# Performance work log

Hardware: AMD Instinct MI355X
Metric: run time of the kernel (lower is better)

Reference implementation:

```python
import jax, jax.numpy as jnp
import numpy as np

T, B, F_, H, D, C = 16, 1024, 512, 128, 8, 100  # trees, batch, feat, hidden, depth, classes
L = 2 ** (D + 1)  # n_leaf = 512


def _routing_tables():
    # Static per-leaf routing: node index and branch side at each depth.
    # Derived from compute_mu's gather indices:
    #   node(d, l) = 2^d - 1 + l // 2^(D+1-d);  side(d, l) = (l // 2^(D-d)) % 2
    l = np.arange(L)
    node = np.stack([(2 ** d - 1) + l // (2 ** (D + 1 - d)) for d in range(D + 1)])  # [D+1, L]
    side = np.stack([(l // (2 ** (D - d))) % 2 for d in range(D + 1)])               # [D+1, L]
    return jnp.asarray(node, dtype=jnp.int32), jnp.asarray(side.astype(np.bool_))


def setup_inputs() -> dict:
    key = jax.random.key(0)
    ks = jax.random.split(key, 4)
    return {
        "feat": jax.random.normal(ks[0], (B, F_), jnp.float32),
        "W1": jax.random.normal(ks[1], (T, F_, H), jnp.float32) * 0.05,
        "b1": jnp.zeros((T, H), jnp.float32),
        "W2": jax.random.normal(ks[2], (T, H, L), jnp.float32) * 0.05,
        "b2": jnp.zeros((T, L), jnp.float32),
        "pi": jax.random.uniform(ks[3], (T, L, C), jnp.float32, -2.0, 2.0),
    }


def reference(feat, W1, b1, W2, b2, pi):
    node, side = _routing_tables()
    # Per-tree MLP head (dropout is identity in eval mode).
    h = jax.nn.relu(jnp.einsum('bf,tfh->tbh', feat, W1) + b1[:, None, :])        # [T,B,H]
    p = jax.nn.sigmoid(jnp.einsum('tbh,thl->tbl', h, W2) + b2[:, None, :])       # [T,B,L]
    # compute_mu: product of routing probs along each root->leaf path.
    sel = p[:, :, node]                          # [T,B,D+1,L] gather (static indices)
    route = jnp.where(side, 1.0 - sel, sel)      # left -> p, right -> 1-p
    mu = jnp.prod(route, axis=2)                 # [T,B,L]
    # compute_py_x: mean over leaves then mean over trees of mu @ softmax(pi).
    leaf_p = jax.nn.softmax(pi, axis=-1)         # [T,L,C]
    py_x = jnp.einsum('tbl,tlc->bc', mu, leaf_p) / (L * T)  # [B,C]
    return jnp.log(py_x)
```

## Files before the change

### kernel.cpp

```cpp
#include <hip/hip_runtime.h>
#include <hip/hip_bf16.h>
#include <math.h>

#define T_ 16
#define B_ 1024
#define F_ 512
#define H_ 128
#define D_ 8
#define C_ 100
#define L_ 512
#define CP_ 112

typedef __attribute__((ext_vector_type(8))) short bf16x8_t;
typedef __attribute__((ext_vector_type(4))) float f32x4_t;

__device__ inline ushort f2bf(float x) {
  __hip_bfloat16 b = __float2bfloat16(x);
  return *(ushort*)&b;
}
__device__ inline float bf2f(ushort u) {
  union { unsigned int i; float f; } v;
  v.i = ((unsigned int)u) << 16;
  return v.f;
}

__device__ inline void bar_raw() {
  asm volatile("" ::: "memory");
  __builtin_amdgcn_s_barrier();
  asm volatile("" ::: "memory");
}
__device__ inline void bar_publish_lds() {
  asm volatile("s_waitcnt lgkmcnt(0)" ::: "memory");
  __builtin_amdgcn_s_barrier();
  asm volatile("" ::: "memory");
}

__global__ __launch_bounds__(256) void k_prep(
    const float* __restrict__ feat, const float* __restrict__ W1,
    const float* __restrict__ W2, const float* __restrict__ pi,
    ushort* __restrict__ feat_bf, ushort* __restrict__ W1T,
    ushort* __restrict__ W2T, ushort* __restrict__ lpT) {
  __shared__ ushort ubuf[112 * 48];
  float (*tile)[33] = (float(*)[33])ubuf;
  ushort (*tileT)[48] = (ushort(*)[48])ubuf;
  const int bid = blockIdx.x, tid = threadIdx.x;

  if (bid < 256) {
    int i = (bid * 256 + tid) * 8;
    float4 a = *(const float4*)(feat + i);
    float4 b = *(const float4*)(feat + i + 4);
    bf16x8_t o;
    o[0] = (short)f2bf(a.x); o[1] = (short)f2bf(a.y);
    o[2] = (short)f2bf(a.z); o[3] = (short)f2bf(a.w);
    o[4] = (short)f2bf(b.x); o[5] = (short)f2bf(b.y);
    o[6] = (short)f2bf(b.z); o[7] = (short)f2bf(b.w);
    *(bf16x8_t*)(feat_bf + i) = o;
    return;
  }
  if (bid < 2304) {
    const float* X; ushort* XT; int K, N, kb, nb, s;
    if (bid < 1280) {
      int r = bid - 256;  kb = r & 15; nb = (r >> 4) & 3;  s = r >> 6;
      X = W1; XT = W1T; K = F_; N = H_;
    } else {
      int r = bid - 1280; kb = r & 3;  nb = (r >> 2) & 15; s = r >> 6;
      X = W2; XT = W2T; K = H_; N = L_;
    }
    const int k0 = kb * 32, n0 = nb * 32;
    const int c = tid & 31, r0 = tid >> 5;
    const float* Xs = X + (size_t)s * K * N;
    ushort* XTs = XT + (size_t)s * N * K;
#pragma unroll
    for (int j = 0; j < 4; ++j)
      tile[r0 + 8 * j][c] = Xs[(size_t)(k0 + r0 + 8 * j) * N + n0 + c];
    __syncthreads();
#pragma unroll
    for (int j = 0; j < 4; ++j)
      XTs[(size_t)(n0 + r0 + 8 * j) * K + k0 + c] = f2bf(tile[c][r0 + 8 * j]);
    return;
  }
  {
    int bid2 = bid - 2304;
    int t = bid2 >> 4, l0 = (bid2 & 15) << 5;
    int lane = tid & 63;
#pragma unroll
    for (int p = 0; p < 8; ++p) {
      int rl = p * 4 + (tid >> 6);
      const float* x = pi + (size_t)(t * L_ + l0 + rl) * C_;
      float v0 = (lane < C_) ? x[lane] : -1e30f;
      float v1 = (lane + 64 < C_) ? x[lane + 64] : -1e30f;
      float m = fmaxf(v0, v1);
#pragma unroll
      for (int off = 32; off; off >>= 1) m = fmaxf(m, __shfl_xor(m, off, 64));
      float e0 = __expf(v0 - m);
      float e1 = (lane + 64 < C_) ? __expf(v1 - m) : 0.0f;
      float sm = e0 + e1;
#pragma unroll
      for (int off = 32; off; off >>= 1) sm += __shfl_xor(sm, off, 64);
      float inv = 1.0f / sm;
      if (lane < C_) tileT[lane][rl] = f2bf(e0 * inv);
      int c2 = lane + 64;
      if (c2 < CP_) tileT[c2][rl] = f2bf(c2 < C_ ? e1 * inv : 0.0f);
    }
    __syncthreads();
    ushort* dst = lpT + (size_t)t * CP_ * L_ + l0;
    for (int idx = tid; idx < 448; idx += 256) {
      int c = idx >> 2, ch = (idx & 3) * 8;
      *(bf16x8_t*)(dst + (size_t)c * L_ + ch) = *(const bf16x8_t*)&tileT[c][ch];
    }
  }
}

__global__ __launch_bounds__(256) void k12_mfma(
    const ushort* __restrict__ feat, const ushort* __restrict__ W1T,
    const float* __restrict__ b1, const ushort* __restrict__ W2T,
    const float* __restrict__ b2, const ushort* __restrict__ lpT,
    float* __restrict__ part) {
  __shared__ ushort smem[29696];
  ushort (*h_s)[136] = (ushort(*)[136])smem;
  ushort (*a_s)[72]  = (ushort(*)[72])(smem + 4352);
  ushort (*b_s)[72]  = (ushort(*)[72])(smem + 6656);
  ushort (*w_s)[136] = (ushort(*)[136])(smem + 4352);
  ushort (*p_s)[520] = (ushort(*)[520])(smem + 13056);

  const int bid = blockIdx.x;
  const int t = bid & 15, b0 = (bid >> 4) * 32;
  const int tid = threadIdx.x;
  const int w = tid >> 6, lane = tid & 63, quad = lane >> 4, n = lane & 15;

  const int arow = tid >> 3, acol = (tid & 7) * 8;
  const ushort* featp = feat + (size_t)(b0 + arow) * F_ + acol;
  const ushort* w1p   = W1T + ((size_t)t * H_ + arow) * F_ + acol;

  {
    f32x4_t acc[2][2];
#pragma unroll
    for (int i = 0; i < 2; ++i)
#pragma unroll
      for (int j = 0; j < 2; ++j) acc[i][j] = (f32x4_t){0.f, 0.f, 0.f, 0.f};

    bf16x8_t ra[2], rb[2][4];
    ra[0] = *(const bf16x8_t*)(featp);
#pragma unroll
    for (int i = 0; i < 4; ++i)
      rb[0][i] = *(const bf16x8_t*)(w1p + (size_t)i * 32 * F_);
    *(bf16x8_t*)&a_s[arow][acol] = ra[0];
#pragma unroll
    for (int i = 0; i < 4; ++i)
      *(bf16x8_t*)&b_s[i * 32 + arow][acol] = rb[0][i];
    bar_publish_lds();
    ra[1] = *(const bf16x8_t*)(featp + 64);
#pragma unroll
    for (int i = 0; i < 4; ++i)
      rb[1][i] = *(const bf16x8_t*)(w1p + (size_t)i * 32 * F_ + 64);
    ra[0] = *(const bf16x8_t*)(featp + 128);
#pragma unroll
    for (int i = 0; i < 4; ++i)
      rb[0][i] = *(const bf16x8_t*)(w1p + (size_t)i * 32 * F_ + 128);

#pragma unroll
    for (int kc = 0; kc < 8; ++kc) {
#pragma unroll
      for (int ks = 0; ks < 64; ks += 32) {
        bf16x8_t af[2], bfr[2];
#pragma unroll
        for (int mt = 0; mt < 2; ++mt)
          af[mt] = *(const bf16x8_t*)&a_s[mt * 16 + n][ks + quad * 8];
#pragma unroll
        for (int nt = 0; nt < 2; ++nt)
          bfr[nt] = *(const bf16x8_t*)&b_s[w * 32 + nt * 16 + n][ks + quad * 8];
#pragma unroll
        for (int mt = 0; mt < 2; ++mt)
#pragma unroll
          for (int nt = 0; nt < 2; ++nt)
            acc[mt][nt] = __builtin_amdgcn_mfma_f32_16x16x32_bf16(
                af[mt], bfr[nt], acc[mt][nt], 0, 0, 0);
      }
      bar_raw();
      if (kc < 7) {
        const int p = (kc + 1) & 1;
        *(bf16x8_t*)&a_s[arow][acol] = ra[p];
#pragma unroll
        for (int i = 0; i < 4; ++i)
          *(bf16x8_t*)&b_s[i * 32 + arow][acol] = rb[p][i];
        bar_publish_lds();
        if (kc < 6) {
          ra[p] = *(const bf16x8_t*)(featp + (kc + 3) * 64);
#pragma unroll
          for (int i = 0; i < 4; ++i)
            rb[p][i] = *(const bf16x8_t*)(w1p + (size_t)i * 32 * F_ + (kc + 3) * 64);
        }
      }
    }
    float bias[2] = {b1[t * H_ + w * 32 + n], b1[t * H_ + w * 32 + 16 + n]};
#pragma unroll
    for (int mt = 0; mt < 2; ++mt)
#pragma unroll
      for (int nt = 0; nt < 2; ++nt)
#pragma unroll
        for (int r = 0; r < 4; ++r) {
          int row = mt * 16 + quad * 4 + r;
          int col = w * 32 + nt * 16 + n;
          float v = acc[mt][nt][r] + bias[nt];
          h_s[row][col] = f2bf(v > 0.f ? v : 0.f);
        }
  }

  {
    const int wrow = tid >> 4, wcol = (tid & 15) * 8;
    const ushort* w2p = W2T + ((size_t)t * L_ + wrow) * H_ + wcol;
    bf16x8_t rw[2][4];
#pragma unroll
    for (int i = 0; i < 4; ++i)
      rw[0][i] = *(const bf16x8_t*)(w2p + (size_t)(i * 16) * H_);
#pragma unroll
    for (int i = 0; i < 4; ++i)
      rw[1][i] = *(const bf16x8_t*)(w2p + (size_t)(64 + i * 16) * H_);
    bar_publish_lds();

    bf16x8_t af2[2][4];
#pragma unroll
    for (int mt = 0; mt < 2; ++mt)
#pragma unroll
      for (int ks = 0; ks < 4; ++ks)
        af2[mt][ks] = *(const bf16x8_t*)&h_s[mt * 16 + n][ks * 32 + quad * 8];
#pragma unroll
    for (int i = 0; i < 4; ++i)
      *(bf16x8_t*)&w_s[i * 16 + wrow][wcol] = rw[0][i];
    bar_publish_lds();
#pragma unroll
    for (int i = 0; i < 4; ++i)
      rw[0][i] = *(const bf16x8_t*)(w2p + (size_t)(128 + i * 16) * H_);

#pragma unroll
    for (int nc = 0; nc < 8; ++nc) {
      f32x4_t acc[2];
      acc[0] = (f32x4_t){0.f, 0.f, 0.f, 0.f};
      acc[1] = (f32x4_t){0.f, 0.f, 0.f, 0.f};
#pragma unroll
      for (int ks = 0; ks < 4; ++ks) {
        bf16x8_t bfrag = *(const bf16x8_t*)&w_s[w * 16 + n][ks * 32 + quad * 8];
        acc[0] = __builtin_amdgcn_mfma_f32_16x16x32_bf16(af2[0][ks], bfrag,
                                                         acc[0], 0, 0, 0);
        acc[1] = __builtin_amdgcn_mfma_f32_16x16x32_bf16(af2[1][ks], bfrag,
                                                         acc[1], 0, 0, 0);
      }
      int l = nc * 64 + w * 16 + n;
      float bias = b2[t * L_ + l];
#pragma unroll
      for (int mt = 0; mt < 2; ++mt)
#pragma unroll
        for (int r = 0; r < 4; ++r) {
          float x = acc[mt][r] + bias;
          p_s[mt * 16 + quad * 4 + r][l] = f2bf(1.0f / (1.0f + __expf(-x)));
        }
      bar_raw();
      if (nc < 7) {
        const int p = (nc + 1) & 1;
#pragma unroll
        for (int i = 0; i < 4; ++i)
          *(bf16x8_t*)&w_s[i * 16 + wrow][wcol] = rw[p][i];
        bar_publish_lds();
        if (nc < 6) {
#pragma unroll
          for (int i = 0; i < 4; ++i)
            rw[p][i] = *(const bf16x8_t*)(w2p + (size_t)((nc + 3) * 64 + i * 16) * H_);
        }
      }
    }
  }
  bar_publish_lds();

  bf16x8_t mo[4][2];
#pragma unroll
  for (int pass = 0; pass < 4; ++pass) {
    int b = pass * 8 + (tid >> 5);
    int s = tid & 31;
    float P = 1.f;
#pragma unroll
    for (int d = 0; d < 5; ++d) {
      int nd = (1 << d) - 1 + (s >> (5 - d));
      int sd = (s >> (4 - d)) & 1;
      float pv = bf2f(p_s[b][nd]);
      P *= sd ? (1.f - pv) : pv;
    }
    float p5 = bf2f(p_s[b][31 + s]);
    float q5[2] = {P * p5, P * (1.f - p5)};
    float q6[4], q7[8];
#pragma unroll
    for (int j = 0; j < 2; ++j) {
      float pv = bf2f(p_s[b][63 + 2 * s + j]);
      q6[2 * j] = q5[j] * pv;
      q6[2 * j + 1] = q5[j] * (1.f - pv);
    }
#pragma unroll
    for (int u = 0; u < 4; ++u) {
      float pv = bf2f(p_s[b][127 + 4 * s + u]);
      q7[2 * u] = q6[u] * pv;
      q7[2 * u + 1] = q6[u] * (1.f - pv);
    }
    bf16x8_t o0, o1;
#pragma unroll
    for (int v = 0; v < 8; ++v) {
      float pv = bf2f(p_s[b][255 + 8 * s + v]);
      ushort e0 = f2bf(q7[v] * pv);
      ushort e1 = f2bf(q7[v] * (1.f - pv));
      if (v < 4) { o0[2 * v] = (short)e0; o0[2 * v + 1] = (short)e1; }
      else       { o1[2 * (v - 4)] = (short)e0; o1[2 * (v - 4) + 1] = (short)e1; }
    }
    mo[pass][0] = o0;
    mo[pass][1] = o1;
  }
  bar_raw();
#pragma unroll
  for (int pass = 0; pass < 4; ++pass) {
    int b = pass * 8 + (tid >> 5);
    int s = tid & 31;
    *(bf16x8_t*)&p_s[b][s * 16]     = mo[pass][0];
    *(bf16x8_t*)&p_s[b][s * 16 + 8] = mo[pass][1];
  }
  bar_publish_lds();

  {
    const int mt = w >> 1;
    const int nt0 = (w & 1) * 4;
    const int ncnt = (w & 1) ? 3 : 4;
    const ushort* arow2 = &p_s[mt * 16 + n][0];
    const ushort* brow = lpT + (size_t)t * CP_ * L_ +
                         ((size_t)(nt0 * 16 + n)) * L_ + quad * 8;
    f32x4_t acc[4];
#pragma unroll
    for (int i = 0; i < 4; ++i) acc[i] = (f32x4_t){0.f, 0.f, 0.f, 0.f};
#pragma unroll 4
    for (int k = 0; k < L_; k += 32) {
      bf16x8_t af = *(const bf16x8_t*)(arow2 + k + quad * 8);
#pragma unroll
      for (int j = 0; j < 4; ++j) {
        if (j < ncnt) {
          bf16x8_t bfr = *(const bf16x8_t*)(brow + (size_t)j * 16 * L_ + k);
          acc[j] = __builtin_amdgcn_mfma_f32_16x16x32_bf16(af, bfr, acc[j],
                                                           0, 0, 0);
        }
      }
    }
    const int m0 = b0 + mt * 16 + quad * 4;
#pragma unroll
    for (int j = 0; j < 4; ++j) {
      int c = (nt0 + j) * 16 + n;
      if (j < ncnt && c < C_) {
#pragma unroll
        for (int r = 0; r < 4; ++r)
          part[((size_t)t * B_ + m0 + r) * C_ + c] = acc[j][r];
      }
    }
  }
}

__global__ __launch_bounds__(256) void k6_log(
    const float* __restrict__ part, float* __restrict__ out) {
  int i = (blockIdx.x * 256 + threadIdx.x) * 4;
  if (i < B_ * C_) {
    float4 s = {0.f, 0.f, 0.f, 0.f};
#pragma unroll
    for (int t = 0; t < T_; ++t) {
      float4 v = *(const float4*)(part + (size_t)t * B_ * C_ + i);
      s.x += v.x; s.y += v.y; s.z += v.z; s.w += v.w;
    }
    const float inv = 1.0f / (L_ * T_);
    float4 o;
    o.x = logf(s.x * inv); o.y = logf(s.y * inv);
    o.z = logf(s.z * inv); o.w = logf(s.w * inv);
    *(float4*)(out + i) = o;
  }
}

extern "C" void kernel_launch(void* const* d_in, const int* in_sizes, int n_in,
                              void* d_out, int out_size, void* d_ws,
                              size_t ws_size, hipStream_t stream) {
  const float* feat = (const float*)d_in[0];
  const float* W1   = (const float*)d_in[1];
  const float* b1   = (const float*)d_in[2];
  const float* W2   = (const float*)d_in[3];
  const float* b2   = (const float*)d_in[4];
  const float* pi   = (const float*)d_in[5];
  float* out = (float*)d_out;

  char* ws = (char*)d_ws;
  ushort* feat_bf  = (ushort*)(ws);
  ushort* W1T_buf  = (ushort*)(ws + ((size_t)1 << 20));
  ushort* W2T_buf  = (ushort*)(ws + ((size_t)3 << 20));
  ushort* lpT_buf  = (ushort*)(ws + ((size_t)5 << 20));
  float*  part_buf = (float*)(ws + ((size_t)7 << 20));

  k_prep<<<2560, 256, 0, stream>>>(feat, W1, W2, pi, feat_bf, W1T_buf,
                                   W2T_buf, lpT_buf);
  k12_mfma<<<512, 256, 0, stream>>>(feat_bf, W1T_buf, b1, W2T_buf, b2,
                                    lpT_buf, part_buf);
  k6_log<<<(B_ * C_ / 4 + 255) / 256, 256, 0, stream>>>(part_buf, out);
}
```

Measured before the change: 109.0 us.

## Double fused MLP-tree kernel block size to 512 threads, redistributing MFMA tiles

The fused kernel now launches 512 threads (8 waves) per block instead of 256, and every phase is re-partitioned. Each wave computes half as many MFMA output tiles in the two MLP GEMMs, the routing-product passes are halved, and the final mu×softmax GEMM gives each wave one or two single 16x16 tiles. The aim is more waves per CU to hide latency and more parallelism per block with 512 blocks on the chip. The cost is less register reuse per wave (fragments are loaded per tile), idle threads during the feat staging, and more waves contending at each barrier.

Result: no change. 108.4 us (-0.5%).

```diff
diff --git a/kernel.cpp b/kernel.cpp
--- a/kernel.cpp
+++ b/kernel.cpp
@@ -111,7 +111,7 @@
   }
 }
 
-__global__ __launch_bounds__(256) void k12_mfma(
+__global__ __launch_bounds__(512, 4) void k12_mfma(
     const ushort* __restrict__ feat, const ushort* __restrict__ W1T,
     const float* __restrict__ b1, const ushort* __restrict__ W2T,
     const float* __restrict__ b2, const ushort* __restrict__ lpT,
@@ -128,154 +128,138 @@
   const int tid = threadIdx.x;
   const int w = tid >> 6, lane = tid & 63, quad = lane >> 4, n = lane & 15;
 
-  const int arow = tid >> 3, acol = (tid & 7) * 8;
-  const ushort* featp = feat + (size_t)(b0 + arow) * F_ + acol;
-  const ushort* w1p   = W1T + ((size_t)t * H_ + arow) * F_ + acol;
+  const bool doA = tid < 256;
+  const int srow = tid >> 3, scol = (tid & 7) * 8;
+  const ushort* featp = feat + (size_t)(b0 + srow) * F_ + scol;
+  const ushort* w1p   = W1T + ((size_t)t * H_ + srow) * F_ + scol;
 
   {
-    f32x4_t acc[2][2];
-#pragma unroll
-    for (int i = 0; i < 2; ++i)
-#pragma unroll
-      for (int j = 0; j < 2; ++j) acc[i][j] = (f32x4_t){0.f, 0.f, 0.f, 0.f};
-
-    bf16x8_t ra[2], rb[2][4];
-    ra[0] = *(const bf16x8_t*)(featp);
-#pragma unroll
-    for (int i = 0; i < 4; ++i)
-      rb[0][i] = *(const bf16x8_t*)(w1p + (size_t)i * 32 * F_);
-    *(bf16x8_t*)&a_s[arow][acol] = ra[0];
-#pragma unroll
-    for (int i = 0; i < 4; ++i)
-      *(bf16x8_t*)&b_s[i * 32 + arow][acol] = rb[0][i];
+    f32x4_t acc[2];
+    acc[0] = (f32x4_t){0.f, 0.f, 0.f, 0.f};
+    acc[1] = (f32x4_t){0.f, 0.f, 0.f, 0.f};
+
+    bf16x8_t ra[2], rb[2][2];
+    if (doA) ra[0] = *(const bf16x8_t*)(featp);
+#pragma unroll
+    for (int i = 0; i < 2; ++i)
+      rb[0][i] = *(const bf16x8_t*)(w1p + (size_t)i * 64 * F_);
+    if (doA) *(bf16x8_t*)&a_s[srow][scol] = ra[0];
+#pragma unroll
+    for (int i = 0; i < 2; ++i)
+      *(bf16x8_t*)&b_s[i * 64 + srow][scol] = rb[0][i];
     bar_publish_lds();
-    ra[1] = *(const bf16x8_t*)(featp + 64);
-#pragma unroll
-    for (int i = 0; i < 4; ++i)
-      rb[1][i] = *(const bf16x8_t*)(w1p + (size_t)i * 32 * F_ + 64);
-    ra[0] = *(const bf16x8_t*)(featp + 128);
-#pragma unroll
-    for (int i = 0; i < 4; ++i)
-      rb[0][i] = *(const bf16x8_t*)(w1p + (size_t)i * 32 * F_ + 128);
+    if (doA) ra[1] = *(const bf16x8_t*)(featp + 64);
+#pragma unroll
+    for (int i = 0; i < 2; ++i)
+      rb[1][i] = *(const bf16x8_t*)(w1p + (size_t)i * 64 * F_ + 64);
+    if (doA) ra[0] = *(const bf16x8_t*)(featp + 128);
+#pragma unroll
+    for (int i = 0; i < 2; ++i)
+      rb[0][i] = *(const bf16x8_t*)(w1p + (size_t)i * 64 * F_ + 128);
 
 #pragma unroll
     for (int kc = 0; kc < 8; ++kc) {
 #pragma unroll
       for (int ks = 0; ks < 64; ks += 32) {
-        bf16x8_t af[2], bfr[2];
-#pragma unroll
-        for (int mt = 0; mt < 2; ++mt)
-          af[mt] = *(const bf16x8_t*)&a_s[mt * 16 + n][ks + quad * 8];
-#pragma unroll
-        for (int nt = 0; nt < 2; ++nt)
-          bfr[nt] = *(const bf16x8_t*)&b_s[w * 32 + nt * 16 + n][ks + quad * 8];
-#pragma unroll
-        for (int mt = 0; mt < 2; ++mt)
-#pragma unroll
-          for (int nt = 0; nt < 2; ++nt)
-            acc[mt][nt] = __builtin_amdgcn_mfma_f32_16x16x32_bf16(
-                af[mt], bfr[nt], acc[mt][nt], 0, 0, 0);
+        bf16x8_t af0 = *(const bf16x8_t*)&a_s[n][ks + quad * 8];
+        bf16x8_t af1 = *(const bf16x8_t*)&a_s[16 + n][ks + quad * 8];
+        bf16x8_t bfr = *(const bf16x8_t*)&b_s[w * 16 + n][ks + quad * 8];
+        acc[0] = __builtin_amdgcn_mfma_f32_16x16x32_bf16(af0, bfr, acc[0],
+                                                         0, 0, 0);
+        acc[1] = __builtin_amdgcn_mfma_f32_16x16x32_bf16(af1, bfr, acc[1],
+                                                         0, 0, 0);
       }
       bar_raw();
       if (kc < 7) {
         const int p = (kc + 1) & 1;
-        *(bf16x8_t*)&a_s[arow][acol] = ra[p];
-#pragma unroll
-        for (int i = 0; i < 4; ++i)
-          *(bf16x8_t*)&b_s[i * 32 + arow][acol] = rb[p][i];
+        if (doA) *(bf16x8_t*)&a_s[srow][scol] = ra[p];
+#pragma unroll
+        for (int i = 0; i < 2; ++i)
+          *(bf16x8_t*)&b_s[i * 64 + srow][scol] = rb[p][i];
         bar_publish_lds();
         if (kc < 6) {
-          ra[p] = *(const bf16x8_t*)(featp + (kc + 3) * 64);
-#pragma unroll
-          for (int i = 0; i < 4; ++i)
-            rb[p][i] = *(const bf16x8_t*)(w1p + (size_t)i * 32 * F_ + (kc + 3) * 64);
+          if (doA) ra[p] = *(const bf16x8_t*)(featp + (kc + 3) * 64);
+#pragma unroll
+          for (int i = 0; i < 2; ++i)
+            rb[p][i] = *(const bf16x8_t*)(w1p + (size_t)i * 64 * F_ + (kc + 3) * 64);
         }
       }
     }
-    float bias[2] = {b1[t * H_ + w * 32 + n], b1[t * H_ + w * 32 + 16 + n]};
+    float bias = b1[t * H_ + w * 16 + n];
 #pragma unroll
     for (int mt = 0; mt < 2; ++mt)
 #pragma unroll
-      for (int nt = 0; nt < 2; ++nt)
-#pragma unroll
-        for (int r = 0; r < 4; ++r) {
-          int row = mt * 16 + quad * 4 + r;
-          int col = w * 32 + nt * 16 + n;
-          float v = acc[mt][nt][r] + bias[nt];
-          h_s[row][col] = f2bf(v > 0.f ? v : 0.f);
-        }
+      for (int r = 0; r < 4; ++r) {
+        int row = mt * 16 + quad * 4 + r;
+        float v = acc[mt][r] + bias;
+        h_s[row][w * 16 + n] = f2bf(v > 0.f ? v : 0.f);
+      }
   }
 
   {
     const int wrow = tid >> 4, wcol = (tid & 15) * 8;
     const ushort* w2p = W2T + ((size_t)t * L_ + wrow) * H_ + wcol;
-    bf16x8_t rw[2][4];
-#pragma unroll
-    for (int i = 0; i < 4; ++i)
-      rw[0][i] = *(const bf16x8_t*)(w2p + (size_t)(i * 16) * H_);
-#pragma unroll
-    for (int i = 0; i < 4; ++i)
-      rw[1][i] = *(const bf16x8_t*)(w2p + (size_t)(64 + i * 16) * H_);
+    bf16x8_t rw[2][2];
+#pragma unroll
+    for (int i = 0; i < 2; ++i)
+      rw[0][i] = *(const bf16x8_t*)(w2p + (size_t)(i * 32) * H_);
+#pragma unroll
+    for (int i = 0; i < 2; ++i)
+      rw[1][i] = *(const bf16x8_t*)(w2p + (size_t)(64 + i * 32) * H_);
     bar_publish_lds();
 
-    bf16x8_t af2[2][4];
-#pragma unroll
-    for (int mt = 0; mt < 2; ++mt)
-#pragma unroll
-      for (int ks = 0; ks < 4; ++ks)
-        af2[mt][ks] = *(const bf16x8_t*)&h_s[mt * 16 + n][ks * 32 + quad * 8];
-#pragma unroll
-    for (int i = 0; i < 4; ++i)
-      *(bf16x8_t*)&w_s[i * 16 + wrow][wcol] = rw[0][i];
+    const int mhalf = w >> 2, lhalf = w & 3;
+    bf16x8_t af2[4];
+#pragma unroll
+    for (int ks = 0; ks < 4; ++ks)
+      af2[ks] = *(const bf16x8_t*)&h_s[mhalf * 16 + n][ks * 32 + quad * 8];
+#pragma unroll
+    for (int i = 0; i < 2; ++i)
+      *(bf16x8_t*)&w_s[i * 32 + wrow][wcol] = rw[0][i];
     bar_publish_lds();
 #pragma unroll
-    for (int i = 0; i < 4; ++i)
-      rw[0][i] = *(const bf16x8_t*)(w2p + (size_t)(128 + i * 16) * H_);
+    for (int i = 0; i < 2; ++i)
+      rw[0][i] = *(const bf16x8_t*)(w2p + (size_t)(128 + i * 32) * H_);
 
 #pragma unroll
     for (int nc = 0; nc < 8; ++nc) {
-      f32x4_t acc[2];
-      acc[0] = (f32x4_t){0.f, 0.f, 0.f, 0.f};
-      acc[1] = (f32x4_t){0.f, 0.f, 0.f, 0.f};
+      f32x4_t acc = (f32x4_t){0.f, 0.f, 0.f, 0.f};
 #pragma unroll
       for (int ks = 0; ks < 4; ++ks) {
-        bf16x8_t bfrag = *(const bf16x8_t*)&w_s[w * 16 + n][ks * 32 + quad * 8];
-        acc[0] = __builtin_amdgcn_mfma_f32_16x16x32_bf16(af2[0][ks], bfrag,
-                                                         acc[0], 0, 0, 0);
-        acc[1] = __builtin_amdgcn_mfma_f32_16x16x32_bf16(af2[1][ks], bfrag,
-                                                         acc[1], 0, 0, 0);
-      }
-      int l = nc * 64 + w * 16 + n;
+        bf16x8_t bfrag = *(const bf16x8_t*)&w_s[lhalf * 16 + n][ks * 32 + quad * 8];
+        acc = __builtin_amdgcn_mfma_f32_16x16x32_bf16(af2[ks], bfrag, acc,
+                                                      0, 0, 0);
+      }
+      int l = nc * 64 + lhalf * 16 + n;
       float bias = b2[t * L_ + l];
 #pragma unroll
-      for (int mt = 0; mt < 2; ++mt)
-#pragma unroll
-        for (int r = 0; r < 4; ++r) {
-          float x = acc[mt][r] + bias;
-          p_s[mt * 16 + quad * 4 + r][l] = f2bf(1.0f / (1.0f + __expf(-x)));
-        }
+      for (int r = 0; r < 4; ++r) {
+        float x = acc[r] + bias;
+        p_s[mhalf * 16 + quad * 4 + r][l] = f2bf(1.0f / (1.0f + __expf(-x)));
+      }
       bar_raw();
       if (nc < 7) {
         const int p = (nc + 1) & 1;
 #pragma unroll
-        for (int i = 0; i < 4; ++i)
-          *(bf16x8_t*)&w_s[i * 16 + wrow][wcol] = rw[p][i];
+        for (int i = 0; i < 2; ++i)
+          *(bf16x8_t*)&w_s[i * 32 + wrow][wcol] = rw[p][i];
         bar_publish_lds();
         if (nc < 6) {
 #pragma unroll
-          for (int i = 0; i < 4; ++i)
-            rw[p][i] = *(const bf16x8_t*)(w2p + (size_t)((nc + 3) * 64 + i * 16) * H_);
+          for (int i = 0; i < 2; ++i)
+            rw[p][i] = *(const bf16x8_t*)(w2p + (size_t)((nc + 3) * 64 + i * 32) * H_);
         }
       }
     }
   }
   bar_publish_lds();
 
-  bf16x8_t mo[4][2];
-#pragma unroll
-  for (int pass = 0; pass < 4; ++pass) {
-    int b = pass * 8 + (tid >> 5);
-    int s = tid & 31;
+  bf16x8_t mo[2][2];
+#pragma unroll
+  for (int pass = 0; pass < 2; ++pass) {
+    int unit = pass * 512 + tid;
+    int b = unit >> 5;
+    int s = unit & 31;
     float P = 1.f;
 #pragma unroll
     for (int d = 0; d < 5; ++d) {
@@ -313,44 +297,38 @@
   }
   bar_raw();
 #pragma unroll
-  for (int pass = 0; pass < 4; ++pass) {
-    int b = pass * 8 + (tid >> 5);
-    int s = tid & 31;
+  for (int pass = 0; pass < 2; ++pass) {
+    int unit = pass * 512 + tid;
+    int b = unit >> 5;
+    int s = unit & 31;
     *(bf16x8_t*)&p_s[b][s * 16]     = mo[pass][0];
     *(bf16x8_t*)&p_s[b][s * 16 + 8] = mo[pass][1];
   }
   bar_publish_lds();
 
   {
-    const int mt = w >> 1;
-    const int nt0 = (w & 1) * 4;
-    const int ncnt = (w & 1) ? 3 : 4;
-    const ushort* arow2 = &p_s[mt * 16 + n][0];
-    const ushort* brow = lpT + (size_t)t * CP_ * L_ +
-                         ((size_t)(nt0 * 16 + n)) * L_ + quad * 8;
-    f32x4_t acc[4];
-#pragma unroll
-    for (int i = 0; i < 4; ++i) acc[i] = (f32x4_t){0.f, 0.f, 0.f, 0.f};
+#pragma unroll
+    for (int uu = 0; uu < 2; ++uu) {
+      int u = w + uu * 8;
+      if (u < 14) {
+        const int mt = u & 1, nt = u >> 1;
+        const ushort* arow = &p_s[mt * 16 + n][0];
+        const ushort* brow = lpT + (size_t)t * CP_ * L_ +
+                             ((size_t)(nt * 16 + n)) * L_ + quad * 8;
+        f32x4_t acc = (f32x4_t){0.f, 0.f, 0.f, 0.f};
 #pragma unroll 4
-    for (int k = 0; k < L_; k += 32) {
-      bf16x8_t af = *(const bf16x8_t*)(arow2 + k + quad * 8);
-#pragma unroll
-      for (int j = 0; j < 4; ++j) {
-        if (j < ncnt) {
-          bf16x8_t bfr = *(const bf16x8_t*)(brow + (size_t)j * 16 * L_ + k);
-          acc[j] = __builtin_amdgcn_mfma_f32_16x16x32_bf16(af, bfr, acc[j],
-                                                           0, 0, 0);
+        for (int k = 0; k < L_; k += 32) {
+          bf16x8_t af = *(const bf16x8_t*)(arow + k + quad * 8);
+          bf16x8_t bfr = *(const bf16x8_t*)(brow + k);
+          acc = __builtin_amdgcn_mfma_f32_16x16x32_bf16(af, bfr, acc, 0, 0, 0);
         }
-      }
-    }
-    const int m0 = b0 + mt * 16 + quad * 4;
-#pragma unroll
-    for (int j = 0; j < 4; ++j) {
-      int c = (nt0 + j) * 16 + n;
-      if (j < ncnt && c < C_) {
-#pragma unroll
-        for (int r = 0; r < 4; ++r)
-          part[((size_t)t * B_ + m0 + r) * C_ + c] = acc[j][r];
+        const int m0 = b0 + mt * 16 + quad * 4;
+        const int c = nt * 16 + n;
+        if (c < C_) {
+#pragma unroll
+          for (int r = 0; r < 4; ++r)
+            part[((size_t)t * B_ + m0 + r) * C_ + c] = acc[r];
+        }
       }
     }
   }
@@ -394,7 +372,7 @@
 
   k_prep<<<2560, 256, 0, stream>>>(feat, W1, W2, pi, feat_bf, W1T_buf,
                                    W2T_buf, lpT_buf);
-  k12_mfma<<<512, 256, 0, stream>>>(feat_bf, W1T_buf, b1, W2T_buf, b2,
+  k12_mfma<<<512, 512, 0, stream>>>(feat_bf, W1T_buf, b1, W2T_buf, b2,
                                     lpT_buf, part_buf);
   k6_log<<<(B_ * C_ / 4 + 255) / 256, 256, 0, stream>>>(part_buf, out);
 }
```
